# Kernel optimization log

Hardware: AMD Instinct MI355X
Metric: run time of the kernel (lower is better)

## Reference

```python
import jax, jax.numpy as jnp
import numpy as np

N = 100000
E = 1600000
IN_C, HID_C, OUT_C = 128, 256, 64
EPS = 1e-5


def _glorot(key, shape):
    fan_in, fan_out = shape
    lim = float(np.sqrt(6.0 / (fan_in + fan_out)))
    return jax.random.uniform(key, shape, jnp.float32, -lim, lim)


def sage_conv(x, src, dst, deg_inv, W_l, b_l, W_r):
    # mean aggregation of neighbor features into target nodes
    msg_sum = jax.ops.segment_sum(x[src], dst, num_segments=N)  # [N, d]
    mean = msg_sum * deg_inv[:, None]
    return mean @ W_l + b_l + x @ W_r


def batch_norm(x, gamma, beta, rm, rv):
    return (x - rm) * jax.lax.rsqrt(rv + EPS) * gamma + beta


def setup_inputs() -> dict:
    key = jax.random.key(0)
    ks = jax.random.split(key, 10)
    x = jax.random.normal(ks[0], (N, IN_C), jnp.float32)
    edge_index = jax.random.randint(ks[1], (2, E), 0, N, jnp.int64)
    inp = {
        "x": x,
        "edge_index": edge_index,
        # layer 1: SAGEConv(IN_C -> HID_C) + BN
        "W1l": _glorot(ks[2], (IN_C, HID_C)),
        "b1l": jnp.zeros((HID_C,), jnp.float32),
        "W1r": _glorot(ks[3], (IN_C, HID_C)),
        "g1": jnp.ones((HID_C,), jnp.float32),
        "be1": jnp.zeros((HID_C,), jnp.float32),
        "rm1": 0.1 * jax.random.normal(ks[4], (HID_C,), jnp.float32),
        "rv1": jnp.ones((HID_C,), jnp.float32),
        # layer 2: SAGEConv(HID_C -> HID_C) + BN
        "W2l": _glorot(ks[5], (HID_C, HID_C)),
        "b2l": jnp.zeros((HID_C,), jnp.float32),
        "W2r": _glorot(ks[6], (HID_C, HID_C)),
        "g2": jnp.ones((HID_C,), jnp.float32),
        "be2": jnp.zeros((HID_C,), jnp.float32),
        "rm2": 0.1 * jax.random.normal(ks[7], (HID_C,), jnp.float32),
        "rv2": jnp.ones((HID_C,), jnp.float32),
        # classifier: SAGEConv(HID_C -> OUT_C)
        "Wcl": _glorot(ks[8], (HID_C, OUT_C)),
        "bcl": jnp.zeros((OUT_C,), jnp.float32),
        "Wcr": _glorot(ks[9], (HID_C, OUT_C)),
    }
    return inp


def reference(x, edge_index, W1l, b1l, W1r, g1, be1, rm1, rv1,
              W2l, b2l, W2r, g2, be2, rm2, rv2, Wcl, bcl, Wcr):
    src, dst = edge_index[0], edge_index[1]
    deg = jax.ops.segment_sum(jnp.ones((E,), jnp.float32), dst, num_segments=N)
    deg_inv = jnp.where(deg > 0, 1.0 / jnp.maximum(deg, 1.0), 0.0)

    h = sage_conv(x, src, dst, deg_inv, W1l, b1l, W1r)
    h = jax.nn.relu(batch_norm(h, g1, be1, rm1, rv1))
    # dropout is identity in eval mode (training=False)
    h = sage_conv(h, src, dst, deg_inv, W2l, b2l, W2r)
    h = jax.nn.relu(batch_norm(h, g2, be2, rm2, rv2))
    return sage_conv(h, src, dst, deg_inv, Wcl, bcl, Wcr)
```

## Files before the change

### kernel.cpp

```cpp
#include <hip/hip_runtime.h>
#include <stdint.h>

#define NN 100000
#define EE 1600000
#define IN_C 128
#define HID_C 256
#define OUT_C 64

#define NB 391
#define CAP 5120
#define K3_NPT 25
#define K3_BLOCKS 250

typedef unsigned short bf16_t;
typedef unsigned int u32;
typedef __attribute__((ext_vector_type(8))) short bf16x8;
typedef __attribute__((ext_vector_type(4))) float f32x4;

__device__ __forceinline__ float b2f(unsigned short u){
  unsigned int x = ((unsigned int)u) << 16;
  return __uint_as_float(x);
}
__device__ __forceinline__ unsigned short f2b(float f){
  unsigned int x = __float_as_uint(f);
  unsigned int r = x + 0x7FFFu + ((x >> 16) & 1u);
  return (unsigned short)(r >> 16);
}

#define GL16(gp, lp) __builtin_amdgcn_global_load_lds( \
    (const __attribute__((address_space(1))) void*)(gp), \
    (__attribute__((address_space(3))) void*)(lp), 16, 0, 0)

__global__ void detect_edge_k(const int* __restrict__ ei, int* __restrict__ eflag){
  __shared__ int sm[256];
  int t = threadIdx.x;
  int o = 0;
  for (int i = t; i < 1024; i += 256) o |= ei[2*i + 1];
  sm[t] = o; __syncthreads();
  for (int s = 128; s > 0; s >>= 1){
    if (t < s) sm[t] |= sm[t + s];
    __syncthreads();
  }
  if (t == 0) *eflag = (sm[0] == 0) ? 1 : 0;
}

__global__ __launch_bounds__(256) void bcount_k(const int* __restrict__ ei,
    const int* __restrict__ eflag, int* __restrict__ bcnt){
  __shared__ int h[NB];
  int t = threadIdx.x;
  for (int i = t; i < NB; i += 256) h[i] = 0;
  __syncthreads();
  int i64 = *eflag;
  int base = blockIdx.x * (256 * K3_NPT);
  #pragma unroll
  for (int q = 0; q < K3_NPT; ++q){
    int e = base + q * 256 + t;
    int d = i64 ? ei[2*(EE + e)] : ei[EE + e];
    atomicAdd(&h[d >> 8], 1);
  }
  __syncthreads();
  for (int i = t; i < NB; i += 256) if (h[i]) atomicAdd(&bcnt[i], h[i]);
}

__global__ void bscan_k(const int* __restrict__ bcnt, int* __restrict__ bbase){
  __shared__ int sm[512];
  int t = threadIdx.x;
  sm[t] = (t < NB) ? bcnt[t] : 0;
  __syncthreads();
  for (int off = 1; off < 512; off <<= 1){
    int a = (t >= off) ? sm[t - off] : 0;
    __syncthreads();
    sm[t] += a;
    __syncthreads();
  }
  if (t <= NB) bbase[t] = (t == 0) ? 0 : sm[t - 1];
}

__global__ __launch_bounds__(256) void bscatter_k(const int* __restrict__ ei,
    const int* __restrict__ eflag, const int* __restrict__ bbase,
    int* __restrict__ bfill, uint2* __restrict__ pairs){
  __shared__ int cnt[NB];
  __shared__ int cnt2[NB];
  __shared__ int lbase[NB];
  int t = threadIdx.x;
  for (int i = t; i < NB; i += 256){ cnt[i] = 0; cnt2[i] = 0; }
  __syncthreads();
  int i64 = *eflag;
  int ebase = blockIdx.x * (256 * K3_NPT);
  int src[K3_NPT], dst[K3_NPT];
  #pragma unroll
  for (int q = 0; q < K3_NPT; ++q){
    int e = ebase + q * 256 + t;
    src[q] = i64 ? ei[2*e] : ei[e];
    dst[q] = i64 ? ei[2*(EE + e)] : ei[EE + e];
    atomicAdd(&cnt[dst[q] >> 8], 1);
  }
  __syncthreads();
  for (int i = t; i < NB; i += 256)
    lbase[i] = cnt[i] ? atomicAdd(&bfill[i], cnt[i]) : 0;
  __syncthreads();
  #pragma unroll
  for (int q = 0; q < K3_NPT; ++q){
    int b = dst[q] >> 8;
    int r = atomicAdd(&cnt2[b], 1);
    pairs[bbase[b] + lbase[b] + r] = make_uint2((u32)src[q], (u32)dst[q]);
  }
}

__global__ __launch_bounds__(256) void bsort_k(const uint2* __restrict__ pairs,
    const int* __restrict__ bbase, int* __restrict__ rowptr, int* __restrict__ csr){
  __shared__ int hist[256];
  __shared__ int pref[257];
  __shared__ int cnt[256];
  __shared__ int lsrc[CAP];
  int b = blockIdx.x;
  int t = threadIdx.x;
  int e0 = bbase[b], e1 = bbase[b + 1];
  int s = e1 - e0;
  hist[t] = 0; cnt[t] = 0;
  __syncthreads();
  for (int i = t; i < s; i += 256)
    atomicAdd(&hist[pairs[e0 + i].y & 255], 1);
  __syncthreads();
  for (int off = 1; off < 256; off <<= 1){
    int a = (t >= off) ? hist[t - off] : 0;
    __syncthreads();
    hist[t] += a;
    __syncthreads();
  }
  if (t == 0) pref[0] = 0;
  pref[t + 1] = hist[t];
  __syncthreads();
  int gid = b * 256 + t;
  if (gid <= NN) rowptr[gid] = e0 + pref[t];
  for (int i = t; i < s; i += 256){
    uint2 p = pairs[e0 + i];
    int bin = p.y & 255;
    int r = atomicAdd(&cnt[bin], 1);
    int pos = pref[bin] + r;
    if (pos < CAP) lsrc[pos] = (int)p.x;
    else           csr[e0 + pos] = (int)p.x;
  }
  __syncthreads();
  int lim = s < CAP ? s : CAP;
  for (int i = t; i < lim; i += 256) csr[e0 + i] = lsrc[i];
}

__global__ __launch_bounds__(256) void xconv_k(const float* __restrict__ x,
    bf16_t* __restrict__ xb, uint8_t* __restrict__ xq, float* __restrict__ scx){
  int row  = (blockIdx.x * 256 + threadIdx.x) >> 6;
  int lane = threadIdx.x & 63;
  if (row >= NN) return;
  float2 u = *(const float2*)(x + (size_t)row * IN_C + lane * 2);
  u32 bb = (u32)f2b(u.x) | ((u32)f2b(u.y) << 16);
  *(u32*)(xb + (size_t)row * IN_C + lane * 2) = bb;
  float m = fmaxf(fabsf(u.x), fabsf(u.y));
  #pragma unroll
  for (int msk = 1; msk < 64; msk <<= 1) m = fmaxf(m, __shfl_xor(m, msk, 64));
  float inv = m > 0.f ? 127.f / m : 0.f;
  float qa = fminf(fmaxf(rintf(u.x * inv), -127.f), 127.f);
  float qb = fminf(fmaxf(rintf(u.y * inv), -127.f), 127.f);
  u32 pa = (u32)(uint8_t)(int8_t)(int)qa | (((u32)(uint8_t)(int8_t)(int)qb) << 8);
  *(unsigned short*)(xq + (size_t)row * IN_C + lane * 2) = (unsigned short)pa;
  if (lane == 0) scx[row] = m / 127.f;
}

struct WtArgs {
  const float* W[6];
  bf16_t* Wt[6];
  int K[6], N[6];
  int off[7];
};

__global__ void wt_all_k(WtArgs a){
  int g = blockIdx.x * 256 + threadIdx.x;
  if (g >= a.off[6]) return;
  #pragma unroll
  for (int s = 0; s < 6; ++s){
    if (g >= a.off[s] && g < a.off[s + 1]){
      int local = g - a.off[s];
      int K = a.K[s], N = a.N[s];
      int n = local / K, k = local - n * K;
      a.Wt[s][local] = f2b(a.W[s][(size_t)k * N + n]);
    }
  }
}

template<int C, bool SIGNED, typename TIN>
__global__ __launch_bounds__(256) void quant_k(const TIN* __restrict__ in,
    uint8_t* __restrict__ outq, float* __restrict__ scales){
  constexpr int V = C / 64;
  int row  = (blockIdx.x * 256 + threadIdx.x) >> 6;
  int lane = threadIdx.x & 63;
  if (row >= NN) return;
  float v[V];
  if constexpr (sizeof(TIN) == 4){
    float2 u = *(const float2*)((const float*)in + (size_t)row * C + lane * 2);
    v[0] = u.x; v[1] = u.y;
  } else {
    const bf16_t* bp = (const bf16_t*)in + (size_t)row * C + lane * V;
    if constexpr (V == 4){
      uint2 u = *(const uint2*)bp;
      v[0] = b2f((unsigned short)(u.x & 0xffffu)); v[1] = b2f((unsigned short)(u.x >> 16));
      v[2] = b2f((unsigned short)(u.y & 0xffffu)); v[3] = b2f((unsigned short)(u.y >> 16));
    } else if constexpr (V == 2){
      u32 u = *(const u32*)bp;
      v[0] = b2f((unsigned short)(u & 0xffffu)); v[1] = b2f((unsigned short)(u >> 16));
    } else {
      v[0] = b2f(*bp);
    }
  }
  float m = 0.f;
  #pragma unroll
  for (int i = 0; i < V; ++i) m = fmaxf(m, SIGNED ? fabsf(v[i]) : v[i]);
  #pragma unroll
  for (int msk = 1; msk < 64; msk <<= 1) m = fmaxf(m, __shfl_xor(m, msk, 64));
  const float qmax = SIGNED ? 127.f : 255.f;
  float inv = m > 0.f ? qmax / m : 0.f;
  uint8_t qb[V];
  #pragma unroll
  for (int i = 0; i < V; ++i){
    float qf = rintf(v[i] * inv);
    if (SIGNED){
      qf = fminf(fmaxf(qf, -127.f), 127.f);
      qb[i] = (uint8_t)(int8_t)(int)qf;
    } else {
      qf = fminf(fmaxf(qf, 0.f), 255.f);
      qb[i] = (uint8_t)(int)qf;
    }
  }
  uint8_t* op = outq + (size_t)row * C + lane * V;
  if constexpr (V == 4){
    u32 p = (u32)qb[0] | ((u32)qb[1] << 8) | ((u32)qb[2] << 16) | ((u32)qb[3] << 24);
    *(u32*)op = p;
  } else if constexpr (V == 2){
    *(unsigned short*)op = (unsigned short)((u32)qb[0] | ((u32)qb[1] << 8));
  } else {
    *op = qb[0];
  }
  if (lane == 0) scales[row] = m / qmax;
}


__device__ __forceinline__ float qdec(u32 w, int b, bool sgn){
  u32 byte = (w >> (8 * b)) & 0xffu;
  return sgn ? (float)(int8_t)byte : (float)byte;
}

template<int C, bool SIGNED>
__global__ __launch_bounds__(256) void agg_q8_k(const uint8_t* __restrict__ tq,
    const float* __restrict__ tsc,
    const int* __restrict__ rowptr, const int* __restrict__ csr,
    bf16_t* __restrict__ outm){
  constexpr int V = C / 64;
  int wid  = (blockIdx.x * 256 + threadIdx.x) >> 6;
  int lane = threadIdx.x & 63;
  if (wid >= NN) return;
  int beg = __builtin_amdgcn_readfirstlane(rowptr[wid]);
  int end = __builtin_amdgcn_readfirstlane(rowptr[wid + 1]);
  float acc[V];
  #pragma unroll
  for (int i = 0; i < V; ++i) acc[i] = 0.f;

  const uint8_t* hb = tq + lane * V;
  int e = beg;
  for (; e + 7 < end; e += 8){
    int   s[8]; float sc[8];
    #pragma unroll
    for (int q = 0; q < 8; ++q) s[q] = csr[e + q];
    u32 w[8];
    #pragma unroll
    for (int q = 0; q < 8; ++q){
      if constexpr (V == 4) w[q] = *(const u32*)(hb + (size_t)s[q] * C);
      else                  w[q] = *(const unsigned short*)(hb + (size_t)s[q] * C);
      sc[q] = tsc[s[q]];
    }
    #pragma unroll
    for (int q = 0; q < 8; ++q)
      #pragma unroll
      for (int i = 0; i < V; ++i)
        acc[i] += sc[q] * qdec(w[q], i, SIGNED);
  }
  for (; e < end; ++e){
    int s0 = csr[e];
    u32 w0;
    if constexpr (V == 4) w0 = *(const u32*)(hb + (size_t)s0 * C);
    else                  w0 = *(const unsigned short*)(hb + (size_t)s0 * C);
    float sc0 = tsc[s0];
    #pragma unroll
    for (int i = 0; i < V; ++i) acc[i] += sc0 * qdec(w0, i, SIGNED);
  }

  int d = end - beg;
  float di = d > 0 ? 1.0f / (float)d : 0.f;
  bf16_t* po = outm + (size_t)wid * C + lane * V;
  if constexpr (V == 2){
    u32 u = (u32)f2b(acc[0] * di) | ((u32)f2b(acc[1] * di) << 16);
    *(u32*)po = u;
  } else {
    uint2 u;
    u.x = (u32)f2b(acc[0] * di) | ((u32)f2b(acc[1] * di) << 16);
    u.y = (u32)f2b(acc[2] * di) | ((u32)f2b(acc[3] * di) << 16);
    *(uint2*)po = u;
  }
}

__global__ __launch_bounds__(256) void agg_final_q8_k(
    const uint8_t* __restrict__ Pq, const float* __restrict__ scp,
    const float* __restrict__ Q,
    const int* __restrict__ rowptr, const int* __restrict__ csr,
    float* __restrict__ out){
  int wid  = (blockIdx.x * 256 + threadIdx.x) >> 6;
  int lane = threadIdx.x & 63;
  if (wid >= NN) return;
  int beg = __builtin_amdgcn_readfirstlane(rowptr[wid]);
  int end = __builtin_amdgcn_readfirstlane(rowptr[wid + 1]);
  const uint8_t* Pb = Pq + lane;
  float acc = 0.f;
  int e = beg;
  for (; e + 7 < end; e += 8){
    int s[8]; uint8_t b[8]; float sc[8];
    #pragma unroll
    for (int q = 0; q < 8; ++q) s[q] = csr[e + q];
    #pragma unroll
    for (int q = 0; q < 8; ++q){ b[q] = Pb[(size_t)s[q] * 64]; sc[q] = scp[s[q]]; }
    #pragma unroll
    for (int q = 0; q < 8; ++q) acc += sc[q] * (float)(int8_t)b[q];
  }
  for (; e < end; ++e) acc += scp[csr[e]] * (float)(int8_t)Pb[(size_t)csr[e] * 64];
  int d = end - beg;
  float di = d > 0 ? 1.0f / (float)d : 0.f;
  out[(size_t)wid * 64 + lane] = acc * di + Q[(size_t)wid * 64 + lane];
}


template<int K_>
__global__ __launch_bounds__(256) void mfma_gemm_k(
    const bf16_t* __restrict__ A0, const bf16_t* __restrict__ A1,
    const bf16_t* __restrict__ W0t, const bf16_t* __restrict__ W1t,
    const float* __restrict__ bias,
    const float* __restrict__ gamma, const float* __restrict__ beta,
    const float* __restrict__ rmean, const float* __restrict__ rvar,
    bf16_t* __restrict__ out, int M, int Nout)
{
  constexpr int BM = 64;
  constexpr int BN = 256;
  constexpr int BK = 64;
  constexpr int KT = K_ / BK;
  constexpr int T  = 2 * KT;
  __shared__ bf16_t As[2][BM * BK];
  __shared__ bf16_t Bs[2][BN * BK];

  int t    = threadIdx.x;
  int lane = t & 63;
  int wid  = t >> 6;
  int l15  = lane & 15;
  int quad = lane >> 4;

  int m0 = blockIdx.x * BM;

  f32x4 acc[4][4];
  #pragma unroll
  for (int i = 0; i < 4; ++i)
    #pragma unroll
    for (int j = 0; j < 4; ++j)
      acc[i][j] = (f32x4){0.f, 0.f, 0.f, 0.f};

  auto stage = [&](int tile, int buf){
    const bf16_t* Ap = (tile < KT) ? A0 : A1;
    const bf16_t* Wp = (tile < KT) ? W0t : W1t;
    int k0 = ((tile < KT) ? tile : tile - KT) * BK;
    #pragma unroll
    for (int i = 0; i < 2; ++i){
      int c   = i * 256 + t;
      int row = c >> 3;
      int k8  = (c & 7) ^ (row & 7);
      int gm  = m0 + row; gm = gm < NN ? gm : NN - 1;
      GL16(Ap + (size_t)gm * K_ + k0 + k8 * 8, &As[buf][(i * 256 + (t & 192)) * 8]);
    }
    #pragma unroll
    for (int i = 0; i < 8; ++i){
      int c   = i * 256 + t;
      int row = c >> 3;
      int k8  = (c & 7) ^ (row & 7);
      GL16(Wp + (size_t)row * K_ + k0 + k8 * 8, &Bs[buf][(i * 256 + (t & 192)) * 8]);
    }
  };

  stage(0, 0);
  #pragma unroll
  for (int tile = 0; tile < T; ++tile){
    int buf = tile & 1;
    if (tile + 1 < T){
      stage(tile + 1, buf ^ 1);
      asm volatile("s_waitcnt vmcnt(10)" ::: "memory");
    } else {
      asm volatile("s_waitcnt vmcnt(0)" ::: "memory");
    }
    __builtin_amdgcn_s_barrier();
    #pragma unroll
    for (int kk = 0; kk < 2; ++kk){
      bf16x8 af[4], bfr[4];
      #pragma unroll
      for (int i = 0; i < 4; ++i){
        int row = i * 16 + l15;
        af[i] = *(const bf16x8*)(&As[buf][(size_t)((row << 3) + ((quad + kk * 4) ^ (row & 7))) * 8]);
      }
      #pragma unroll
      for (int j = 0; j < 4; ++j){
        int row = wid * 64 + j * 16 + l15;
        bfr[j] = *(const bf16x8*)(&Bs[buf][(size_t)((row << 3) + ((quad + kk * 4) ^ (row & 7))) * 8]);
      }
      #pragma unroll
      for (int i = 0; i < 4; ++i)
        #pragma unroll
        for (int j = 0; j < 4; ++j)
          acc[i][j] = __builtin_amdgcn_mfma_f32_16x16x32_bf16(af[i], bfr[j], acc[i][j], 0, 0, 0);
    }
    __builtin_amdgcn_s_barrier();
  }

  #pragma unroll
  for (int j = 0; j < 4; ++j){
    int col = wid * 64 + j * 16 + l15;
    float sc = gamma[col] * rsqrtf(rvar[col] + 1e-5f);
    float shift = (bias[col] - rmean[col]) * sc + beta[col];
    #pragma unroll
    for (int i = 0; i < 4; ++i){
      int rbase = m0 + i * 16 + quad * 4;
      #pragma unroll
      for (int r = 0; r < 4; ++r){
        int row = rbase + r;
        if (row < M){
          float v = fmaxf(acc[i][j][r] * sc + shift, 0.f);
          out[(size_t)row * Nout + col] = f2b(v);
        }
      }
    }
  }
}


__global__ __launch_bounds__(256) void gemm3_k(
    const bf16_t* __restrict__ A, const bf16_t* __restrict__ Wt,
    const float* __restrict__ bcl,
    uint8_t* __restrict__ Pq, float* __restrict__ scp,
    float* __restrict__ Q, int M)
{
  constexpr int K_ = 256, BM = 64, BN = 128, BK = 64;
  constexpr int T = K_ / BK;
  __shared__ bf16_t As[2][BM * BK];
  __shared__ bf16_t Bs[2][BN * BK];

  int t    = threadIdx.x;
  int lane = t & 63;
  int wid  = t >> 6;
  int wr   = wid >> 1, wc = wid & 1;
  int l15  = lane & 15;
  int quad = lane >> 4;
  int m0 = blockIdx.x * BM;

  f32x4 acc[2][4];
  #pragma unroll
  for (int i = 0; i < 2; ++i)
    #pragma unroll
    for (int j = 0; j < 4; ++j)
      acc[i][j] = (f32x4){0.f, 0.f, 0.f, 0.f};

  auto stage = [&](int tile, int buf){
    int k0 = tile * BK;
    #pragma unroll
    for (int i = 0; i < 2; ++i){
      int c   = i * 256 + t;
      int row = c >> 3;
      int k8  = (c & 7) ^ (row & 7);
      int gm  = m0 + row; gm = gm < NN ? gm : NN - 1;
      GL16(A + (size_t)gm * K_ + k0 + k8 * 8, &As[buf][(i * 256 + (t & 192)) * 8]);
    }
    #pragma unroll
    for (int i = 0; i < 4; ++i){
      int c   = i * 256 + t;
      int row = c >> 3;
      int k8  = (c & 7) ^ (row & 7);
      GL16(Wt + (size_t)row * K_ + k0 + k8 * 8, &Bs[buf][(i * 256 + (t & 192)) * 8]);
    }
  };

  stage(0, 0);
  #pragma unroll
  for (int tile = 0; tile < T; ++tile){
    int buf = tile & 1;
    if (tile + 1 < T){
      stage(tile + 1, buf ^ 1);
      asm volatile("s_waitcnt vmcnt(6)" ::: "memory");
    } else {
      asm volatile("s_waitcnt vmcnt(0)" ::: "memory");
    }
    __builtin_amdgcn_s_barrier();
    #pragma unroll
    for (int kk = 0; kk < 2; ++kk){
      bf16x8 af[2], bfr[4];
      #pragma unroll
      for (int i = 0; i < 2; ++i){
        int row = wr * 32 + i * 16 + l15;
        af[i] = *(const bf16x8*)(&As[buf][(size_t)((row << 3) + ((quad + kk * 4) ^ (row & 7))) * 8]);
      }
      #pragma unroll
      for (int j = 0; j < 4; ++j){
        int row = wc * 64 + j * 16 + l15;
        bfr[j] = *(const bf16x8*)(&Bs[buf][(size_t)((row << 3) + ((quad + kk * 4) ^ (row & 7))) * 8]);
      }
      #pragma unroll
      for (int i = 0; i < 2; ++i)
        #pragma unroll
        for (int j = 0; j < 4; ++j)
          acc[i][j] = __builtin_amdgcn_mfma_f32_16x16x32_bf16(af[i], bfr[j], acc[i][j], 0, 0, 0);
    }
    __builtin_amdgcn_s_barrier();
  }

  if (wc == 0){
    #pragma unroll
    for (int i = 0; i < 2; ++i){
      #pragma unroll
      for (int r = 0; r < 4; ++r){
        int row = m0 + wr * 32 + i * 16 + quad * 4 + r;
        float m = 0.f;
        #pragma unroll
        for (int j = 0; j < 4; ++j) m = fmaxf(m, fabsf(acc[i][j][r]));
        #pragma unroll
        for (int msk = 1; msk < 16; msk <<= 1) m = fmaxf(m, __shfl_xor(m, msk, 64));
        float inv = m > 0.f ? 127.f / m : 0.f;
        if (row < M){
          #pragma unroll
          for (int j = 0; j < 4; ++j){
            float qf = fminf(fmaxf(rintf(acc[i][j][r] * inv), -127.f), 127.f);
            ((int8_t*)Pq)[(size_t)row * 64 + j * 16 + l15] = (int8_t)(int)qf;
          }
          if (l15 == 0) scp[row] = m / 127.f;
        }
      }
    }
  } else {
    #pragma unroll
    for (int j = 0; j < 4; ++j){
      int col = j * 16 + l15;
      float bc = bcl[col];
      #pragma unroll
      for (int i = 0; i < 2; ++i){
        int rbase = m0 + wr * 32 + i * 16 + quad * 4;
        #pragma unroll
        for (int r = 0; r < 4; ++r){
          int row = rbase + r;
          if (row < M) Q[(size_t)row * 64 + col] = acc[i][j][r] + bc;
        }
      }
    }
  }
}


extern "C" void kernel_launch(void* const* d_in, const int* in_sizes, int n_in,
                              void* d_out, int out_size, void* d_ws, size_t ws_size,
                              hipStream_t stream)
{
  const float* x   = (const float*)d_in[0];
  const int*   ei  = (const int*)d_in[1];
  const float* W1l = (const float*)d_in[2];
  const float* b1l = (const float*)d_in[3];
  const float* W1r = (const float*)d_in[4];
  const float* g1  = (const float*)d_in[5];
  const float* be1 = (const float*)d_in[6];
  const float* rm1 = (const float*)d_in[7];
  const float* rv1 = (const float*)d_in[8];
  const float* W2l = (const float*)d_in[9];
  const float* b2l = (const float*)d_in[10];
  const float* W2r = (const float*)d_in[11];
  const float* g2  = (const float*)d_in[12];
  const float* be2 = (const float*)d_in[13];
  const float* rm2 = (const float*)d_in[14];
  const float* rv2 = (const float*)d_in[15];
  const float* Wcl = (const float*)d_in[16];
  const float* bcl = (const float*)d_in[17];
  const float* Wcr = (const float*)d_in[18];
  (void)in_sizes; (void)n_in; (void)out_size; (void)ws_size;

  char* ws = (char*)d_ws;
  size_t off = 0;
  auto alloc = [&](size_t bytes)->char* {
    char* p = ws + off;
    off += (bytes + 15) & ~(size_t)15;
    return p;
  };
  int*    bcnt   = (int*)   alloc(800 * 4);
  int*    bfill  = bcnt + 400;
  int*    bbase  = (int*)   alloc((size_t)(NB + 1) * 4);
  int*    rowptr = (int*)   alloc((size_t)(NN + 1) * 4);
  int*    eflag  = (int*)   alloc(16);
  int*    csr    = (int*)   alloc((size_t)EE * 4);
  bf16_t* xb     = (bf16_t*)alloc((size_t)NN * IN_C * 2);
  bf16_t* aggb   = (bf16_t*)alloc((size_t)NN * HID_C * 2);
  bf16_t* h1     = (bf16_t*)alloc((size_t)NN * HID_C * 2);
  bf16_t* h2     = (bf16_t*)alloc((size_t)NN * HID_C * 2);
  bf16_t* W1lt   = (bf16_t*)alloc((size_t)IN_C  * HID_C * 2);
  bf16_t* W1rt   = (bf16_t*)alloc((size_t)IN_C  * HID_C * 2);
  bf16_t* W2lt   = (bf16_t*)alloc((size_t)HID_C * HID_C * 2);
  bf16_t* W2rt   = (bf16_t*)alloc((size_t)HID_C * HID_C * 2);
  bf16_t* Wc3t   = (bf16_t*)alloc((size_t)128 * HID_C * 2);
  float*  sc1    = (float*) alloc((size_t)NN * 4);
  float*  scp    = (float*) alloc((size_t)NN * 4);

  uint2*   pairs = (uint2*)aggb;
  uint8_t* xq  = (uint8_t*)h2;
  float*   scx = (float*)((char*)h2 + (size_t)NN * IN_C);
  uint8_t* h1q = (uint8_t*)xb;
  uint8_t* Pq  = (uint8_t*)aggb;
  float*   Q   = (float*)h1;

  hipMemsetAsync(bcnt, 0, 800 * 4, stream);

  int wb = (NN + 3) / 4;
  int g64 = (NN + 63) / 64;

  xconv_k<<<wb, 256, 0, stream>>>(x, xb, xq, scx);

  WtArgs wa;
  wa.W[0] = W1l; wa.Wt[0] = W1lt; wa.K[0] = IN_C;  wa.N[0] = HID_C;
  wa.W[1] = W1r; wa.Wt[1] = W1rt; wa.K[1] = IN_C;  wa.N[1] = HID_C;
  wa.W[2] = W2l; wa.Wt[2] = W2lt; wa.K[2] = HID_C; wa.N[2] = HID_C;
  wa.W[3] = W2r; wa.Wt[3] = W2rt; wa.K[3] = HID_C; wa.N[3] = HID_C;
  wa.W[4] = Wcl; wa.Wt[4] = Wc3t;             wa.K[4] = HID_C; wa.N[4] = OUT_C;
  wa.W[5] = Wcr; wa.Wt[5] = Wc3t + 64 * 256;  wa.K[5] = HID_C; wa.N[5] = OUT_C;
  wa.off[0] = 0;
  for (int s = 0; s < 6; ++s) wa.off[s + 1] = wa.off[s] + wa.K[s] * wa.N[s];
  wt_all_k<<<(wa.off[6] + 255) / 256, 256, 0, stream>>>(wa);

  detect_edge_k<<<1, 256, 0, stream>>>(ei, eflag);
  bcount_k<<<K3_BLOCKS, 256, 0, stream>>>(ei, eflag, bcnt);
  bscan_k<<<1, 512, 0, stream>>>(bcnt, bbase);
  bscatter_k<<<K3_BLOCKS, 256, 0, stream>>>(ei, eflag, bbase, bfill, pairs);
  bsort_k<<<NB, 256, 0, stream>>>(pairs, bbase, rowptr, csr);

  agg_q8_k<IN_C, true><<<wb, 256, 0, stream>>>(xq, scx, rowptr, csr, aggb);
  mfma_gemm_k<IN_C><<<g64, 256, 0, stream>>>(
      aggb, xb, W1lt, W1rt, b1l, g1, be1, rm1, rv1, h1, NN, HID_C);

  quant_k<HID_C, false, bf16_t><<<wb, 256, 0, stream>>>(h1, h1q, sc1);
  agg_q8_k<HID_C, false><<<wb, 256, 0, stream>>>(h1q, sc1, rowptr, csr, aggb);
  mfma_gemm_k<HID_C><<<g64, 256, 0, stream>>>(
      aggb, h1, W2lt, W2rt, b2l, g2, be2, rm2, rv2, h2, NN, HID_C);

  gemm3_k<<<g64, 256, 0, stream>>>(h2, Wc3t, bcl, Pq, scp, Q, NN);
  agg_final_q8_k<<<wb, 256, 0, stream>>>(Pq, scp, Q, rowptr, csr, (float*)d_out);
}
```

Measured before the change: 542.4 us.

## Fuse h1 uint8 quantization into layer-1 GEMM epilogue and inline edge-format detection

The layer-1 GEMM epilogue now computes per-row max across the four waves through shared memory, quantizes the post-ReLU activations to uint8 in an LDS tile and writes them out with per-row scales. This removes the separate quant_k pass, which re-read h1 from global memory. The one-block detect_edge_k launch is also dropped, and each bcount/bscatter block redoes the small int64-format detection itself. The cost is extra LDS traffic and barriers in the GEMM epilogue, plus redundant detection reads in every block of the two edge kernels.

```diff
diff --git a/kernel.cpp b/kernel.cpp
--- a/kernel.cpp
+++ b/kernel.cpp
@@ -31,26 +31,22 @@
     (const __attribute__((address_space(1))) void*)(gp), \
     (__attribute__((address_space(3))) void*)(lp), 16, 0, 0)
 
-__global__ void detect_edge_k(const int* __restrict__ ei, int* __restrict__ eflag){
-  __shared__ int sm[256];
+
+__global__ __launch_bounds__(256) void bcount_k(const int* __restrict__ ei,
+    int* __restrict__ bcnt){
+  __shared__ int h[NB];
   int t = threadIdx.x;
   int o = 0;
   for (int i = t; i < 1024; i += 256) o |= ei[2*i + 1];
-  sm[t] = o; __syncthreads();
+  h[t] = o; __syncthreads();
   for (int s = 128; s > 0; s >>= 1){
-    if (t < s) sm[t] |= sm[t + s];
-    __syncthreads();
-  }
-  if (t == 0) *eflag = (sm[0] == 0) ? 1 : 0;
-}
-
-__global__ __launch_bounds__(256) void bcount_k(const int* __restrict__ ei,
-    const int* __restrict__ eflag, int* __restrict__ bcnt){
-  __shared__ int h[NB];
-  int t = threadIdx.x;
+    if (t < s) h[t] |= h[t + s];
+    __syncthreads();
+  }
+  int i64 = (h[0] == 0) ? 1 : 0;
+  __syncthreads();
   for (int i = t; i < NB; i += 256) h[i] = 0;
   __syncthreads();
-  int i64 = *eflag;
   int base = blockIdx.x * (256 * K3_NPT);
   #pragma unroll
   for (int q = 0; q < K3_NPT; ++q){
@@ -77,15 +73,23 @@
 }
 
 __global__ __launch_bounds__(256) void bscatter_k(const int* __restrict__ ei,
-    const int* __restrict__ eflag, const int* __restrict__ bbase,
+    const int* __restrict__ bbase,
     int* __restrict__ bfill, uint2* __restrict__ pairs){
   __shared__ int cnt[NB];
   __shared__ int cnt2[NB];
   __shared__ int lbase[NB];
   int t = threadIdx.x;
+  int o = 0;
+  for (int i = t; i < 1024; i += 256) o |= ei[2*i + 1];
+  cnt[t] = o; __syncthreads();
+  for (int s = 128; s > 0; s >>= 1){
+    if (t < s) cnt[t] |= cnt[t + s];
+    __syncthreads();
+  }
+  int i64 = (cnt[0] == 0) ? 1 : 0;
+  __syncthreads();
   for (int i = t; i < NB; i += 256){ cnt[i] = 0; cnt2[i] = 0; }
   __syncthreads();
-  int i64 = *eflag;
   int ebase = blockIdx.x * (256 * K3_NPT);
   int src[K3_NPT], dst[K3_NPT];
   #pragma unroll
@@ -184,61 +188,6 @@
       a.Wt[s][local] = f2b(a.W[s][(size_t)k * N + n]);
     }
   }
-}
-
-template<int C, bool SIGNED, typename TIN>
-__global__ __launch_bounds__(256) void quant_k(const TIN* __restrict__ in,
-    uint8_t* __restrict__ outq, float* __restrict__ scales){
-  constexpr int V = C / 64;
-  int row  = (blockIdx.x * 256 + threadIdx.x) >> 6;
-  int lane = threadIdx.x & 63;
-  if (row >= NN) return;
-  float v[V];
-  if constexpr (sizeof(TIN) == 4){
-    float2 u = *(const float2*)((const float*)in + (size_t)row * C + lane * 2);
-    v[0] = u.x; v[1] = u.y;
-  } else {
-    const bf16_t* bp = (const bf16_t*)in + (size_t)row * C + lane * V;
-    if constexpr (V == 4){
-      uint2 u = *(const uint2*)bp;
-      v[0] = b2f((unsigned short)(u.x & 0xffffu)); v[1] = b2f((unsigned short)(u.x >> 16));
-      v[2] = b2f((unsigned short)(u.y & 0xffffu)); v[3] = b2f((unsigned short)(u.y >> 16));
-    } else if constexpr (V == 2){
-      u32 u = *(const u32*)bp;
-      v[0] = b2f((unsigned short)(u & 0xffffu)); v[1] = b2f((unsigned short)(u >> 16));
-    } else {
-      v[0] = b2f(*bp);
-    }
-  }
-  float m = 0.f;
-  #pragma unroll
-  for (int i = 0; i < V; ++i) m = fmaxf(m, SIGNED ? fabsf(v[i]) : v[i]);
-  #pragma unroll
-  for (int msk = 1; msk < 64; msk <<= 1) m = fmaxf(m, __shfl_xor(m, msk, 64));
-  const float qmax = SIGNED ? 127.f : 255.f;
-  float inv = m > 0.f ? qmax / m : 0.f;
-  uint8_t qb[V];
-  #pragma unroll
-  for (int i = 0; i < V; ++i){
-    float qf = rintf(v[i] * inv);
-    if (SIGNED){
-      qf = fminf(fmaxf(qf, -127.f), 127.f);
-      qb[i] = (uint8_t)(int8_t)(int)qf;
-    } else {
-      qf = fminf(fmaxf(qf, 0.f), 255.f);
-      qb[i] = (uint8_t)(int)qf;
-    }
-  }
-  uint8_t* op = outq + (size_t)row * C + lane * V;
-  if constexpr (V == 4){
-    u32 p = (u32)qb[0] | ((u32)qb[1] << 8) | ((u32)qb[2] << 16) | ((u32)qb[3] << 24);
-    *(u32*)op = p;
-  } else if constexpr (V == 2){
-    *(unsigned short*)op = (unsigned short)((u32)qb[0] | ((u32)qb[1] << 8));
-  } else {
-    *op = qb[0];
-  }
-  if (lane == 0) scales[row] = m / qmax;
 }
 
 
@@ -334,14 +283,16 @@
 }
 
 
-template<int K_>
+template<int K_, bool QUANT>
 __global__ __launch_bounds__(256) void mfma_gemm_k(
     const bf16_t* __restrict__ A0, const bf16_t* __restrict__ A1,
     const bf16_t* __restrict__ W0t, const bf16_t* __restrict__ W1t,
     const float* __restrict__ bias,
     const float* __restrict__ gamma, const float* __restrict__ beta,
     const float* __restrict__ rmean, const float* __restrict__ rvar,
-    bf16_t* __restrict__ out, int M, int Nout)
+    bf16_t* __restrict__ out,
+    uint8_t* __restrict__ outq, float* __restrict__ oscales,
+    int M, int Nout)
 {
   constexpr int BM = 64;
   constexpr int BN = 256;
@@ -426,16 +377,67 @@
     float sc = gamma[col] * rsqrtf(rvar[col] + 1e-5f);
     float shift = (bias[col] - rmean[col]) * sc + beta[col];
     #pragma unroll
+    for (int i = 0; i < 4; ++i)
+      #pragma unroll
+      for (int r = 0; r < 4; ++r)
+        acc[i][j][r] = fmaxf(acc[i][j][r] * sc + shift, 0.f);
+  }
+  #pragma unroll
+  for (int j = 0; j < 4; ++j){
+    int col = wid * 64 + j * 16 + l15;
+    #pragma unroll
     for (int i = 0; i < 4; ++i){
       int rbase = m0 + i * 16 + quad * 4;
       #pragma unroll
       for (int r = 0; r < 4; ++r){
         int row = rbase + r;
-        if (row < M){
-          float v = fmaxf(acc[i][j][r] * sc + shift, 0.f);
-          out[(size_t)row * Nout + col] = f2b(v);
+        if (row < M) out[(size_t)row * Nout + col] = f2b(acc[i][j][r]);
+      }
+    }
+  }
+
+  if constexpr (QUANT){
+    float*   wmax  = (float*)As;
+    uint8_t* qtile = (uint8_t*)Bs;
+    #pragma unroll
+    for (int i = 0; i < 4; ++i){
+      #pragma unroll
+      for (int r = 0; r < 4; ++r){
+        float m = fmaxf(fmaxf(acc[i][0][r], acc[i][1][r]),
+                        fmaxf(acc[i][2][r], acc[i][3][r]));
+        #pragma unroll
+        for (int msk = 1; msk < 16; msk <<= 1) m = fmaxf(m, __shfl_xor(m, msk, 64));
+        if (l15 == 0) wmax[wid * 64 + i * 16 + quad * 4 + r] = m;
+      }
+    }
+    __syncthreads();
+    #pragma unroll
+    for (int i = 0; i < 4; ++i){
+      #pragma unroll
+      for (int r = 0; r < 4; ++r){
+        int rl = i * 16 + quad * 4 + r;
+        float m = fmaxf(fmaxf(wmax[rl], wmax[64 + rl]),
+                        fmaxf(wmax[128 + rl], wmax[192 + rl]));
+        float inv = m > 0.f ? 255.f / m : 0.f;
+        #pragma unroll
+        for (int j = 0; j < 4; ++j){
+          float qf = fminf(rintf(acc[i][j][r] * inv), 255.f);
+          qtile[rl * 256 + wid * 64 + j * 16 + l15] = (uint8_t)(int)qf;
         }
-      }
+        if (wid == 0 && l15 == 0){
+          int row = m0 + rl;
+          if (row < M) oscales[row] = m * (1.f / 255.f);
+        }
+      }
+    }
+    __syncthreads();
+    int rl  = t >> 2;
+    int co  = (t & 3) * 64;
+    int row = m0 + rl;
+    if (row < M){
+      const uint4* src = (const uint4*)(qtile + rl * 256 + co);
+      uint4* dst = (uint4*)(outq + (size_t)row * 256 + co);
+      dst[0] = src[0]; dst[1] = src[1]; dst[2] = src[2]; dst[3] = src[3];
     }
   }
 }
@@ -596,7 +598,6 @@
   int*    bfill  = bcnt + 400;
   int*    bbase  = (int*)   alloc((size_t)(NB + 1) * 4);
   int*    rowptr = (int*)   alloc((size_t)(NN + 1) * 4);
-  int*    eflag  = (int*)   alloc(16);
   int*    csr    = (int*)   alloc((size_t)EE * 4);
   bf16_t* xb     = (bf16_t*)alloc((size_t)NN * IN_C * 2);
   bf16_t* aggb   = (bf16_t*)alloc((size_t)NN * HID_C * 2);
@@ -635,20 +636,18 @@
   for (int s = 0; s < 6; ++s) wa.off[s + 1] = wa.off[s] + wa.K[s] * wa.N[s];
   wt_all_k<<<(wa.off[6] + 255) / 256, 256, 0, stream>>>(wa);
 
-  detect_edge_k<<<1, 256, 0, stream>>>(ei, eflag);
-  bcount_k<<<K3_BLOCKS, 256, 0, stream>>>(ei, eflag, bcnt);
+  bcount_k<<<K3_BLOCKS, 256, 0, stream>>>(ei, bcnt);
   bscan_k<<<1, 512, 0, stream>>>(bcnt, bbase);
-  bscatter_k<<<K3_BLOCKS, 256, 0, stream>>>(ei, eflag, bbase, bfill, pairs);
+  bscatter_k<<<K3_BLOCKS, 256, 0, stream>>>(ei, bbase, bfill, pairs);
   bsort_k<<<NB, 256, 0, stream>>>(pairs, bbase, rowptr, csr);
 
   agg_q8_k<IN_C, true><<<wb, 256, 0, stream>>>(xq, scx, rowptr, csr, aggb);
-  mfma_gemm_k<IN_C><<<g64, 256, 0, stream>>>(
-      aggb, xb, W1lt, W1rt, b1l, g1, be1, rm1, rv1, h1, NN, HID_C);
-
-  quant_k<HID_C, false, bf16_t><<<wb, 256, 0, stream>>>(h1, h1q, sc1);
+  mfma_gemm_k<IN_C, true><<<g64, 256, 0, stream>>>(
+      aggb, xb, W1lt, W1rt, b1l, g1, be1, rm1, rv1, h1, h1q, sc1, NN, HID_C);
+
   agg_q8_k<HID_C, false><<<wb, 256, 0, stream>>>(h1q, sc1, rowptr, csr, aggb);
-  mfma_gemm_k<HID_C><<<g64, 256, 0, stream>>>(
-      aggb, h1, W2lt, W2rt, b2l, g2, be2, rm2, rv2, h2, NN, HID_C);
+  mfma_gemm_k<HID_C, false><<<g64, 256, 0, stream>>>(
+      aggb, h1, W2lt, W2rt, b2l, g2, be2, rm2, rv2, h2, nullptr, nullptr, NN, HID_C);
 
   gemm3_k<<<g64, 256, 0, stream>>>(h2, Wc3t, bcl, Pq, scp, Q, NN);
   agg_final_q8_k<<<wb, 256, 0, stream>>>(Pq, scp, Q, rowptr, csr, (float*)d_out);
```

New measurement: 553.0 us. About the same (+1.9%).
